# Kernel optimization log

Hardware: AMD Instinct MI355X
Metric: run time of the kernel (lower is better)

## Reference

```python
import jax, jax.numpy as jnp
import numpy as np
from jax import lax

HID = 896          # hidden_size
HALF = HID // 2    # 448
BINS = 256         # 2 ** (bits/2), bits=16
B, T = 16, 2048


def setup_inputs() -> dict:
    key = jax.random.key(0)
    ks = jax.random.split(key, 16)
    rn = lambda k, shape, s: (jax.random.normal(k, shape, jnp.float32) * s)
    inp = {
        'conditional': jax.random.normal(ks[0], (B, T, 3, HID), jnp.float32),
        'input_signal': jax.random.randint(ks[1], (B, T, 2), 0, BINS, jnp.int32),
        'target_coarse': jax.random.randint(ks[2], (B, T, 1), 0, BINS, jnp.int32),
        # project_coarse_input: Linear(2, 3*half, bias=False)
        'Wc': rn(ks[3], (2, 3 * HALF), 0.5),
        # project_fine_input: Linear(3, 3*half, bias=False)
        'Wf': rn(ks[4], (3, 3 * HALF), 0.5),
        # stripped GRU hidden-to-hidden weights/biases (input projection is rnn_input itself)
        'W_hh': rn(ks[5], (HID, 3 * HID), 0.02),
        'b_ih': jnp.zeros((3 * HID,), jnp.float32),
        'b_hh': jnp.zeros((3 * HID,), jnp.float32),
        # to_bins_coarse: Linear(half, half) + ReLU + Linear(half, bins)
        'W1c': rn(ks[6], (HALF, HALF), 0.05), 'b1c': jnp.zeros((HALF,), jnp.float32),
        'W2c': rn(ks[7], (HALF, BINS), 0.05), 'b2c': jnp.zeros((BINS,), jnp.float32),
        # to_bins_fine
        'W1f': rn(ks[8], (HALF, HALF), 0.05), 'b1f': jnp.zeros((HALF,), jnp.float32),
        'W2f': rn(ks[9], (HALF, BINS), 0.05), 'b2f': jnp.zeros((BINS,), jnp.float32),
    }
    return inp


def _scale(x):
    # [0, BINS-1] -> [-1, 1]
    return x.astype(jnp.float32) / ((BINS - 1) / 2.0) - 1.0


def reference(conditional, input_signal, target_coarse, Wc, Wf, W_hh, b_ih, b_hh,
              W1c, b1c, W2c, b2c, W1f, b1f, W2f, b2f):
    sig = _scale(input_signal)          # [B, T, 2]
    tc = _scale(target_coarse)          # [B, T, 1]

    coarse_proj = (sig @ Wc).reshape(B, T, 3, HALF)
    fine_proj = (jnp.concatenate([sig, tc], axis=2) @ Wf).reshape(B, T, 3, HALF)
    # concat along feature halves -> [B, T, 3, HID], add conditional, flatten gates
    rnn_input = jnp.concatenate([coarse_proj, fine_proj], axis=3) + conditional
    rnn_input = rnn_input.reshape(B, T, 3 * HID) + b_ih
    xs = rnn_input.transpose(1, 0, 2)   # [T, B, 3*HID]

    def step(h, x_t):
        gh = h @ W_hh + b_hh                      # [B, 3*HID]
        xr, xz, xn = jnp.split(x_t, 3, axis=-1)
        hr, hz, hn = jnp.split(gh, 3, axis=-1)
        r = jax.nn.sigmoid(xr + hr)
        z = jax.nn.sigmoid(xz + hz)
        n = jnp.tanh(xn + r * hn)
        h_new = (1.0 - z) * n + z * h
        return h_new, h_new

    h0 = jnp.zeros((B, HID), jnp.float32)
    last_hidden, hidden_states = lax.scan(step, h0, xs)   # [T, B, HID]
    hidden_states = hidden_states.transpose(1, 0, 2)      # [B, T, HID]

    hidden_coarse = hidden_states[..., :HALF]
    # NOTE: original code applies to_bins_fine to hidden_coarse as well (faithful).
    out_coarse = jax.nn.relu(hidden_coarse @ W1c + b1c) @ W2c + b2c
    out_fine = jax.nn.relu(hidden_coarse @ W1f + b1f) @ W2f + b2f
    return out_coarse, out_fine, last_hidden
```

## Files before the change

kernel.cpp:

```cpp
#include <hip/hip_runtime.h>
#include <hip/hip_cooperative_groups.h>

namespace cg = cooperative_groups;

#define BB 16
#define TT 2048
#define HIDN 896
#define HALFN 448
#define NBINS 256
#define NWG 112
#define NTHR 64
#define WSTR 904

typedef __attribute__((ext_vector_type(8))) short short8;
typedef __attribute__((ext_vector_type(4))) float f32x4;
typedef __attribute__((ext_vector_type(2))) unsigned long long ull2;

__device__ __forceinline__ unsigned short f2bf(float x) {
    unsigned int u = __float_as_uint(x);
    unsigned int r = u + 0x7FFFu + ((u >> 16) & 1u);
    return (unsigned short)(r >> 16);
}

__global__ __launch_bounds__(NTHR, 1)
void scan_kernel(const float* __restrict__ cond,
                 const int*   __restrict__ sig,
                 const int*   __restrict__ tcrs,
                 const float* __restrict__ Wc,
                 const float* __restrict__ Wf,
                 const float* __restrict__ Whh,
                 const float* __restrict__ b_ih,
                 const float* __restrict__ b_hh,
                 unsigned long long* __restrict__ hx,
                 int* __restrict__ slots,
                 unsigned short* __restrict__ hc_out,
                 float* __restrict__ lasth)
{
    __shared__ unsigned short sW[32 * WSTR];

    const int tid  = threadIdx.x;
    const int wg   = blockIdx.x;
    const int cb   = (wg & 7) * 14 + (wg >> 3);
    const int col0 = cb * 8;

    for (int idx = tid; idx < 32 * HIDN; idx += NTHR) {
        int j2 = idx & 31, k = idx >> 5;
        unsigned short wv = 0;
        if (j2 < 16)
            wv = f2bf(Whh[(size_t)k * 2688 + (j2 >> 3) * HIDN + col0 + (j2 & 7)]);
        else if (j2 < 24)
            wv = f2bf(Whh[(size_t)k * 2688 + 2 * HIDN + col0 + (j2 & 7)]);
        sW[j2 * WSTR + k] = wv;
    }
    if (tid == 0)
        __hip_atomic_store(&slots[wg * 16], 0, __ATOMIC_RELAXED, __HIP_MEMORY_SCOPE_AGENT);

    const int l  = tid;
    const int q  = l & 15;
    const int hi = l >> 4;
    const int gA   = q >> 3;
    const int colA = col0 + (q & 7);

    float wpA0, wpA1, wpA2, wpB0, wpB1, wpB2;
    if (colA < HALFN) {
        wpA0 = Wc[gA * HALFN + colA];
        wpA1 = Wc[1344 + gA * HALFN + colA];
        wpA2 = 0.f;
        wpB0 = Wc[2 * HALFN + colA];
        wpB1 = Wc[1344 + 2 * HALFN + colA];
        wpB2 = 0.f;
    } else {
        int ck = colA - HALFN;
        wpA0 = Wf[gA * HALFN + ck];
        wpA1 = Wf[1344 + gA * HALFN + ck];
        wpA2 = Wf[2688 + gA * HALFN + ck];
        wpB0 = Wf[2 * HALFN + ck];
        wpB1 = Wf[1344 + 2 * HALFN + ck];
        wpB2 = Wf[2688 + 2 * HALFN + ck];
    }
    const float biA = b_ih[gA * HIDN + colA];
    const float bhA = b_hh[gA * HIDN + colA];
    const float biB = b_ih[2 * HIDN + colA];
    const float bhB = b_hh[2 * HIDN + colA];

    float hp[4] = {0.f, 0.f, 0.f, 0.f};

    float xcA[4], xcB[4];
    int   si0[4], si1[4], si2[4];

#define PREFETCH(tt) {                                                         \
    int tn_ = (tt) < TT ? (tt) : TT - 1;                                       \
    _Pragma("unroll")                                                          \
    for (int r_ = 0; r_ < 4; ++r_) {                                           \
        size_t bt_ = (size_t)(hi * 4 + r_) * TT + tn_;                         \
        xcA[r_] = cond[(bt_ * 3 + gA) * HIDN + colA];                          \
        xcB[r_] = cond[(bt_ * 3 + 2) * HIDN + colA];                           \
        si0[r_] = sig[bt_ * 2 + 0];                                            \
        si1[r_] = sig[bt_ * 2 + 1];                                            \
        si2[r_] = tcrs[bt_];                                                   \
    } }

    PREFETCH(0);

    __syncthreads();
    cg::this_grid().sync();

    const float inv = 1.f / 127.5f;
    const int zsrc = (l & 48) | 8 | (q & 7);

#define WAITALL(t) { bool ok_;                                                 \
    for (;;) {                                                                 \
        int a_ = __hip_atomic_load(&slots[l * 16],                             \
            __ATOMIC_RELAXED, __HIP_MEMORY_SCOPE_AGENT);                       \
        int b_ = (l < 48) ? __hip_atomic_load(&slots[(l + 64) * 16],           \
            __ATOMIC_RELAXED, __HIP_MEMORY_SCOPE_AGENT) : a_;                  \
        ok_ = (a_ >= (t)) & (b_ >= (t));                                       \
        if (__all(ok_)) break;                                                 \
        __builtin_amdgcn_s_sleep(1);                                           \
    }                                                                          \
    asm volatile("" ::: "memory"); }

#define LOADH(s, V) _Pragma("unroll")                                          \
    for (int i_ = 0; i_ < 7; ++i_) {                                           \
        _Pragma("unroll")                                                      \
        for (int h_ = 0; h_ < 2; ++h_)                                         \
            V[2*i_ + h_] = __hip_atomic_load(                                  \
                &hb[(size_t)(4 * ((s)*7 + i_) + hi) * 32 + h_ * 16 + q],       \
                __ATOMIC_RELAXED, __HIP_MEMORY_SCOPE_AGENT);                   \
    }

#define MFMAS(s, V) _Pragma("unroll")                                          \
    for (int i_ = 0; i_ < 7; ++i_) {                                           \
        ull2 tv_; tv_.x = V[2*i_]; tv_.y = V[2*i_ + 1];                        \
        short8 av_ = __builtin_bit_cast(short8, tv_);                          \
        int ks_ = (s)*7 + i_;                                                  \
        short8 b1_ = *(const short8*)&sW[q * WSTR + hi * 8 + ks_ * 32];        \
        chA[ks_ & 3] = __builtin_amdgcn_mfma_f32_16x16x32_bf16(                \
            av_, b1_, chA[ks_ & 3], 0, 0, 0);                                  \
        short8 b2_ = *(const short8*)&sW[(16 + q) * WSTR + hi * 8 + ks_ * 32]; \
        chB[ks_ & 3] = __builtin_amdgcn_mfma_f32_16x16x32_bf16(                \
            av_, b2_, chB[ks_ & 3], 0, 0, 0);                                  \
    }

    for (int t = 0; t < TT; ++t) {
        f32x4 chA[4] = {}, chB[4] = {};
        if (t > 0) {
            WAITALL(t);
            const unsigned long long* hb = hx + (size_t)(t & 1) * 3584;
            unsigned long long va[14], vb[14];
            LOADH(0, va);
            LOADH(1, vb);
            MFMAS(0, va);
            LOADH(2, va);
            MFMAS(1, vb);
            LOADH(3, vb);
            MFMAS(2, va);
            MFMAS(3, vb);
        }
        f32x4 aA = (chA[0] + chA[1]) + (chA[2] + chA[3]);
        f32x4 aB = (chB[0] + chB[1]) + (chB[2] + chB[3]);

        float xvB[4], sigA[4];
        #pragma unroll
        for (int r = 0; r < 4; ++r) {
            float g0 = (float)si0[r] * inv - 1.f;
            float g1 = (float)si1[r] * inv - 1.f;
            float g2 = (float)si2[r] * inv - 1.f;
            float xvA = xcA[r] + biA + g0*wpA0 + g1*wpA1 + g2*wpA2;
            xvB[r]    = xcB[r] + biB + g0*wpB0 + g1*wpB1 + g2*wpB2;
            sigA[r] = 1.f / (1.f + __expf(-(xvA + aA[r] + bhA)));
        }
        float hnv[4];
        unsigned short hbits[4] = {0, 0, 0, 0};
        #pragma unroll
        for (int r = 0; r < 4; ++r) {
            float zz = __shfl(sigA[r], zsrc);
            float a2v = xvB[r] + sigA[r] * (aB[r] + bhB);
            float e = __expf(-2.f * a2v);
            float n = (1.f - e) / (1.f + e);
            float hn = (1.f - zz) * n + zz * hp[r];
            hnv[r] = hn;
            if (q < 8) { hp[r] = hn; hbits[r] = f2bf(hn); }
        }
        if (t == TT - 1 && q < 8) {
            #pragma unroll
            for (int r = 0; r < 4; ++r)
                lasth[(size_t)(hi * 4 + r) * HIDN + colA] = hnv[r];
        }

        unsigned p32[4];
        unsigned long long hv64[4];
        #pragma unroll
        for (int r = 0; r < 4; ++r) {
            int o1 = __shfl_xor((int)(unsigned)hbits[r], 1);
            p32[r] = ((unsigned)hbits[r] & 0xffffu) | ((unsigned)o1 << 16);
            int o2 = __shfl_xor((int)p32[r], 2);
            hv64[r] = (unsigned long long)p32[r] |
                      ((unsigned long long)(unsigned)o2 << 32);
        }
        if (t < TT - 1 && (q == 0 || q == 4)) {
            unsigned long long* hd = hx + (size_t)((t + 1) & 1) * 3584;
            #pragma unroll
            for (int r = 0; r < 4; ++r)
                __hip_atomic_store(&hd[(size_t)cb * 32 + (q >> 2) * 16 + hi * 4 + r],
                                   hv64[r], __ATOMIC_RELAXED, __HIP_MEMORY_SCOPE_AGENT);
        }
        asm volatile("s_waitcnt vmcnt(0)" ::: "memory");
        if (tid == 0)
            __hip_atomic_store(&slots[wg * 16], t + 1,
                               __ATOMIC_RELAXED, __HIP_MEMORY_SCOPE_AGENT);

        PREFETCH(t + 1);
        if (cb < 56 && q < 8 && !(q & 1)) {
            unsigned* hc32 = (unsigned*)hc_out;
            #pragma unroll
            for (int r = 0; r < 4; ++r)
                hc32[((size_t)(hi * 4 + r) * TT + t) * 224 + cb * 4 + (q >> 1)] = p32[r];
        }
    }
#undef WAITALL
#undef LOADH
#undef MFMAS
#undef PREFETCH
}

template<int RELU_BF16>
__global__ __launch_bounds__(256)
void head_gemm(const unsigned short* __restrict__ A,
               const float* __restrict__ Bw,
               const float* __restrict__ bias,
               unsigned short* __restrict__ Cb,
               float* __restrict__ Cf,
               int N)
{
    const int K = 448;
    __shared__ float As[32][68];
    __shared__ float Bs[32][68];
    const int tid = threadIdx.x;
    const int tx = tid & 15;
    const int ty = tid >> 4;
    const int bm = blockIdx.x * 64;
    const int bn = blockIdx.y * 64;

    float acc[4][4] = {};

    for (int k0 = 0; k0 < K; k0 += 32) {
        #pragma unroll
        for (int it = 0; it < 2; ++it) {
            int idx = tid + it * 256;
            int m   = idx >> 3;
            int k4  = idx & 7;
            ushort4 av = *(const ushort4*)(A + (size_t)(bm + m) * K + k0 + k4 * 4);
            As[k4 * 4 + 0][m] = __uint_as_float((unsigned)av.x << 16);
            As[k4 * 4 + 1][m] = __uint_as_float((unsigned)av.y << 16);
            As[k4 * 4 + 2][m] = __uint_as_float((unsigned)av.z << 16);
            As[k4 * 4 + 3][m] = __uint_as_float((unsigned)av.w << 16);
        }
        #pragma unroll
        for (int it = 0; it < 2; ++it) {
            int idx = tid + it * 256;
            int k   = idx >> 4;
            int n4  = idx & 15;
            *(float4*)&Bs[k][n4 * 4] =
                *(const float4*)(Bw + (size_t)(k0 + k) * N + bn + n4 * 4);
        }
        __syncthreads();
        #pragma unroll
        for (int k = 0; k < 32; ++k) {
            float4 a4 = *(float4*)&As[k][ty * 4];
            float4 b4 = *(float4*)&Bs[k][tx * 4];
            float ar[4] = {a4.x, a4.y, a4.z, a4.w};
            float br[4] = {b4.x, b4.y, b4.z, b4.w};
            #pragma unroll
            for (int i = 0; i < 4; ++i)
                #pragma unroll
                for (int j = 0; j < 4; ++j)
                    acc[i][j] = fmaf(ar[i], br[j], acc[i][j]);
        }
        __syncthreads();
    }

    float4 bsv = *(const float4*)(bias + bn + tx * 4);
    float bb[4] = {bsv.x, bsv.y, bsv.z, bsv.w};
    #pragma unroll
    for (int i = 0; i < 4; ++i) {
        int row = bm + ty * 4 + i;
        float v[4];
        #pragma unroll
        for (int j = 0; j < 4; ++j) v[j] = acc[i][j] + bb[j];
        if (RELU_BF16) {
            ushort4 o;
            o.x = f2bf(fmaxf(v[0], 0.f));
            o.y = f2bf(fmaxf(v[1], 0.f));
            o.z = f2bf(fmaxf(v[2], 0.f));
            o.w = f2bf(fmaxf(v[3], 0.f));
            *(ushort4*)(Cb + (size_t)row * N + bn + tx * 4) = o;
        } else {
            float4 o = make_float4(v[0], v[1], v[2], v[3]);
            *(float4*)(Cf + (size_t)row * N + bn + tx * 4) = o;
        }
    }
}

extern "C" void kernel_launch(void* const* d_in, const int* in_sizes, int n_in,
                              void* d_out, int out_size, void* d_ws, size_t ws_size,
                              hipStream_t stream)
{
    const float* cond = (const float*)d_in[0];
    const int*   sig  = (const int*)d_in[1];
    const int*   tcrs = (const int*)d_in[2];
    const float* Wc   = (const float*)d_in[3];
    const float* Wf   = (const float*)d_in[4];
    const float* Whh  = (const float*)d_in[5];
    const float* bih  = (const float*)d_in[6];
    const float* bhh  = (const float*)d_in[7];
    const float* W1c  = (const float*)d_in[8];
    const float* b1c  = (const float*)d_in[9];
    const float* W2c  = (const float*)d_in[10];
    const float* b2c  = (const float*)d_in[11];
    const float* W1f  = (const float*)d_in[12];
    const float* b1f  = (const float*)d_in[13];
    const float* W2f  = (const float*)d_in[14];
    const float* b2f  = (const float*)d_in[15];

    char* ws = (char*)d_ws;
    int* slots               = (int*)ws;
    unsigned long long* hx   = (unsigned long long*)(ws + 8192);
    unsigned short* hc       = (unsigned short*)(ws + 65536);
    unsigned short* hid1     = (unsigned short*)(ws + 65536 + 29360128);

    float* outc  = (float*)d_out;
    float* outf  = outc + (size_t)BB * TT * NBINS;
    float* lasth = outc + 2 * (size_t)BB * TT * NBINS;

    void* args[] = {(void*)&cond, (void*)&sig, (void*)&tcrs, (void*)&Wc, (void*)&Wf,
                    (void*)&Whh, (void*)&bih, (void*)&bhh,
                    (void*)&hx, (void*)&slots, (void*)&hc, (void*)&lasth};
    hipLaunchCooperativeKernel((void*)scan_kernel, dim3(NWG), dim3(NTHR),
                               args, 0, stream);

    dim3 blk(256);
    head_gemm<1><<<dim3(512, 7), blk, 0, stream>>>(hc,   W1c, b1c, hid1, nullptr, 448);
    head_gemm<0><<<dim3(512, 4), blk, 0, stream>>>(hid1, W2c, b2c, nullptr, outc, 256);
    head_gemm<1><<<dim3(512, 7), blk, 0, stream>>>(hc,   W1f, b1f, hid1, nullptr, 448);
    head_gemm<0><<<dim3(512, 4), blk, 0, stream>>>(hid1, W2f, b2f, nullptr, outf, 256);
}
```

Baseline: 8.093 ms.

## Use parity-split atomic counter barrier and MFMA bf16 head GEMMs

Replaces the per-workgroup slot flags, which every wave polled (112 loads plus a wave vote), with two global counters indexed by step parity. Each workgroup does a fetch_add after publishing its hidden slice, and waiters spin on a single load until the count reaches 112 times the step index. Separately, the head GEMMs move from scalar fp32 FMA to bf16 MFMA 16x16x32 with 128-row tiles, with the weights converted to bf16 in shared memory. Atomic contention on one address may add latency, and bf16 weights in the head lower precision.

```diff
diff --git a/kernel.cpp b/kernel.cpp
--- a/kernel.cpp
+++ b/kernel.cpp
@@ -32,7 +32,7 @@
                  const float* __restrict__ b_ih,
                  const float* __restrict__ b_hh,
                  unsigned long long* __restrict__ hx,
-                 int* __restrict__ slots,
+                 unsigned* __restrict__ ctr,
                  unsigned short* __restrict__ hc_out,
                  float* __restrict__ lasth)
 {
@@ -52,8 +52,10 @@
             wv = f2bf(Whh[(size_t)k * 2688 + 2 * HIDN + col0 + (j2 & 7)]);
         sW[j2 * WSTR + k] = wv;
     }
-    if (tid == 0)
-        __hip_atomic_store(&slots[wg * 16], 0, __ATOMIC_RELAXED, __HIP_MEMORY_SCOPE_AGENT);
+    if (wg == 0 && tid == 0) {
+        __hip_atomic_store(&ctr[0],  0u, __ATOMIC_RELAXED, __HIP_MEMORY_SCOPE_AGENT);
+        __hip_atomic_store(&ctr[16], 0u, __ATOMIC_RELAXED, __HIP_MEMORY_SCOPE_AGENT);
+    }
 
     const int l  = tid;
     const int q  = l & 15;
@@ -108,14 +110,12 @@
     const float inv = 1.f / 127.5f;
     const int zsrc = (l & 48) | 8 | (q & 7);
 
-#define WAITALL(t) { bool ok_;                                                 \
+#define WAITCTR(t) {                                                           \
+    const unsigned tgt_ = 112u * (unsigned)(((t) + 1) >> 1);                   \
     for (;;) {                                                                 \
-        int a_ = __hip_atomic_load(&slots[l * 16],                             \
+        unsigned c_ = __hip_atomic_load(&ctr[((t) & 1) * 16],                  \
             __ATOMIC_RELAXED, __HIP_MEMORY_SCOPE_AGENT);                       \
-        int b_ = (l < 48) ? __hip_atomic_load(&slots[(l + 64) * 16],           \
-            __ATOMIC_RELAXED, __HIP_MEMORY_SCOPE_AGENT) : a_;                  \
-        ok_ = (a_ >= (t)) & (b_ >= (t));                                       \
-        if (__all(ok_)) break;                                                 \
+        if (c_ >= tgt_) break;                                                 \
         __builtin_amdgcn_s_sleep(1);                                           \
     }                                                                          \
     asm volatile("" ::: "memory"); }
@@ -145,7 +145,7 @@
     for (int t = 0; t < TT; ++t) {
         f32x4 chA[4] = {}, chB[4] = {};
         if (t > 0) {
-            WAITALL(t);
+            WAITCTR(t);
             const unsigned long long* hb = hx + (size_t)(t & 1) * 3584;
             unsigned long long va[14], vb[14];
             LOADH(0, va);
@@ -207,8 +207,8 @@
         }
         asm volatile("s_waitcnt vmcnt(0)" ::: "memory");
         if (tid == 0)
-            __hip_atomic_store(&slots[wg * 16], t + 1,
-                               __ATOMIC_RELAXED, __HIP_MEMORY_SCOPE_AGENT);
+            __hip_atomic_fetch_add(&ctr[((t + 1) & 1) * 16], 1u,
+                                   __ATOMIC_RELAXED, __HIP_MEMORY_SCOPE_AGENT);
 
         PREFETCH(t + 1);
         if (cb < 56 && q < 8 && !(q & 1)) {
@@ -218,7 +218,7 @@
                 hc32[((size_t)(hi * 4 + r) * TT + t) * 224 + cb * 4 + (q >> 1)] = p32[r];
         }
     }
-#undef WAITALL
+#undef WAITCTR
 #undef LOADH
 #undef MFMAS
 #undef PREFETCH
@@ -234,70 +234,66 @@
                int N)
 {
     const int K = 448;
-    __shared__ float As[32][68];
-    __shared__ float Bs[32][68];
+    __shared__ unsigned short sA[128 * 40];
+    __shared__ unsigned short sBt[64 * 40];
     const int tid = threadIdx.x;
-    const int tx = tid & 15;
-    const int ty = tid >> 4;
-    const int bm = blockIdx.x * 64;
-    const int bn = blockIdx.y * 64;
-
-    float acc[4][4] = {};
+    const int w   = tid >> 6;
+    const int l   = tid & 63;
+    const int wm  = (w >> 1) * 64;
+    const int wn  = (w & 1) * 32;
+    const int bm  = blockIdx.x * 128;
+    const int bn  = blockIdx.y * 64;
+
+    f32x4 acc[4][2] = {};
 
     for (int k0 = 0; k0 < K; k0 += 32) {
         #pragma unroll
         for (int it = 0; it < 2; ++it) {
             int idx = tid + it * 256;
-            int m   = idx >> 3;
-            int k4  = idx & 7;
-            ushort4 av = *(const ushort4*)(A + (size_t)(bm + m) * K + k0 + k4 * 4);
-            As[k4 * 4 + 0][m] = __uint_as_float((unsigned)av.x << 16);
-            As[k4 * 4 + 1][m] = __uint_as_float((unsigned)av.y << 16);
-            As[k4 * 4 + 2][m] = __uint_as_float((unsigned)av.z << 16);
-            As[k4 * 4 + 3][m] = __uint_as_float((unsigned)av.w << 16);
+            int row = idx >> 2;
+            int ck  = (idx & 3) * 8;
+            *(float4*)&sA[row * 40 + ck] =
+                *(const float4*)(A + (size_t)(bm + row) * K + k0 + ck);
         }
         #pragma unroll
         for (int it = 0; it < 2; ++it) {
             int idx = tid + it * 256;
-            int k   = idx >> 4;
-            int n4  = idx & 15;
-            *(float4*)&Bs[k][n4 * 4] =
-                *(const float4*)(Bw + (size_t)(k0 + k) * N + bn + n4 * 4);
+            int kk = idx >> 4;
+            int c4 = (idx & 15) * 4;
+            float4 v = *(const float4*)(Bw + (size_t)(k0 + kk) * N + bn + c4);
+            sBt[(c4 + 0) * 40 + kk] = f2bf(v.x);
+            sBt[(c4 + 1) * 40 + kk] = f2bf(v.y);
+            sBt[(c4 + 2) * 40 + kk] = f2bf(v.z);
+            sBt[(c4 + 3) * 40 + kk] = f2bf(v.w);
         }
         __syncthreads();
-        #pragma unroll
-        for (int k = 0; k < 32; ++k) {
-            float4 a4 = *(float4*)&As[k][ty * 4];
-            float4 b4 = *(float4*)&Bs[k][tx * 4];
-            float ar[4] = {a4.x, a4.y, a4.z, a4.w};
-            float br[4] = {b4.x, b4.y, b4.z, b4.w};
+        const int kq = (l >> 4) * 8;
+        short8 bv0 = *(const short8*)&sBt[(wn + (l & 15)) * 40 + kq];
+        short8 bv1 = *(const short8*)&sBt[(wn + 16 + (l & 15)) * 40 + kq];
+        #pragma unroll
+        for (int rb = 0; rb < 4; ++rb) {
+            short8 av = *(const short8*)&sA[(wm + rb * 16 + (l & 15)) * 40 + kq];
+            acc[rb][0] = __builtin_amdgcn_mfma_f32_16x16x32_bf16(av, bv0, acc[rb][0], 0, 0, 0);
+            acc[rb][1] = __builtin_amdgcn_mfma_f32_16x16x32_bf16(av, bv1, acc[rb][1], 0, 0, 0);
+        }
+        __syncthreads();
+    }
+
+    #pragma unroll
+    for (int rb = 0; rb < 4; ++rb) {
+        #pragma unroll
+        for (int cbk = 0; cbk < 2; ++cbk) {
+            int col = bn + wn + cbk * 16 + (l & 15);
+            float bv = bias[col];
             #pragma unroll
-            for (int i = 0; i < 4; ++i)
-                #pragma unroll
-                for (int j = 0; j < 4; ++j)
-                    acc[i][j] = fmaf(ar[i], br[j], acc[i][j]);
-        }
-        __syncthreads();
-    }
-
-    float4 bsv = *(const float4*)(bias + bn + tx * 4);
-    float bb[4] = {bsv.x, bsv.y, bsv.z, bsv.w};
-    #pragma unroll
-    for (int i = 0; i < 4; ++i) {
-        int row = bm + ty * 4 + i;
-        float v[4];
-        #pragma unroll
-        for (int j = 0; j < 4; ++j) v[j] = acc[i][j] + bb[j];
-        if (RELU_BF16) {
-            ushort4 o;
-            o.x = f2bf(fmaxf(v[0], 0.f));
-            o.y = f2bf(fmaxf(v[1], 0.f));
-            o.z = f2bf(fmaxf(v[2], 0.f));
-            o.w = f2bf(fmaxf(v[3], 0.f));
-            *(ushort4*)(Cb + (size_t)row * N + bn + tx * 4) = o;
-        } else {
-            float4 o = make_float4(v[0], v[1], v[2], v[3]);
-            *(float4*)(Cf + (size_t)row * N + bn + tx * 4) = o;
+            for (int j = 0; j < 4; ++j) {
+                int row = bm + wm + rb * 16 + (l >> 4) * 4 + j;
+                float v = acc[rb][cbk][j] + bv;
+                if (RELU_BF16)
+                    Cb[(size_t)row * N + col] = f2bf(fmaxf(v, 0.f));
+                else
+                    Cf[(size_t)row * N + col] = v;
+            }
         }
     }
 }
@@ -324,7 +320,7 @@
     const float* b2f  = (const float*)d_in[15];
 
     char* ws = (char*)d_ws;
-    int* slots               = (int*)ws;
+    unsigned* ctr            = (unsigned*)ws;
     unsigned long long* hx   = (unsigned long long*)(ws + 8192);
     unsigned short* hc       = (unsigned short*)(ws + 65536);
     unsigned short* hid1     = (unsigned short*)(ws + 65536 + 29360128);
@@ -335,13 +331,13 @@
 
     void* args[] = {(void*)&cond, (void*)&sig, (void*)&tcrs, (void*)&Wc, (void*)&Wf,
                     (void*)&Whh, (void*)&bih, (void*)&bhh,
-                    (void*)&hx, (void*)&slots, (void*)&hc, (void*)&lasth};
+                    (void*)&hx, (void*)&ctr, (void*)&hc, (void*)&lasth};
     hipLaunchCooperativeKernel((void*)scan_kernel, dim3(NWG), dim3(NTHR),
                                args, 0, stream);
 
     dim3 blk(256);
-    head_gemm<1><<<dim3(512, 7), blk, 0, stream>>>(hc,   W1c, b1c, hid1, nullptr, 448);
-    head_gemm<0><<<dim3(512, 4), blk, 0, stream>>>(hid1, W2c, b2c, nullptr, outc, 256);
-    head_gemm<1><<<dim3(512, 7), blk, 0, stream>>>(hc,   W1f, b1f, hid1, nullptr, 448);
-    head_gemm<0><<<dim3(512, 4), blk, 0, stream>>>(hid1, W2f, b2f, nullptr, outf, 256);
+    head_gemm<1><<<dim3(256, 7), blk, 0, stream>>>(hc,   W1c, b1c, hid1, nullptr, 448);
+    head_gemm<0><<<dim3(256, 4), blk, 0, stream>>>(hid1, W2c, b2c, nullptr, outc, 256);
+    head_gemm<1><<<dim3(256, 7), blk, 0, stream>>>(hc,   W1f, b1f, hid1, nullptr, 448);
+    head_gemm<0><<<dim3(256, 4), blk, 0, stream>>>(hid1, W2f, b2f, nullptr, outf, 256);
 }
```

After: 8.967 ms. 10.8% more time.
